# Kernel optimization log

Measured on AMD Instinct MI355X. Metric: run time of the kernel, lower is better.

Reference implementation:

```python
import jax, jax.numpy as jnp
import numpy as np

# SemiConv2d with semifield_type='MaxMin':
#   out[n,oc,i,j] = max_{ic,kh,kw} min(x_pad[n,ic,i+kh,j+kw], kernel[oc,ic,kh,kw])
# stride=1, 'same' padding with -inf (identity of max).

def setup_inputs() -> dict:
    key = jax.random.key(0)
    kx, kk = jax.random.split(key)
    x = jax.random.normal(kx, (8, 32, 96, 96), dtype=jnp.float32)
    kernel = jax.random.normal(kk, (32, 32, 3, 3), dtype=jnp.float32)
    return {"x": x, "kernel": kernel}


def reference(x, kernel):
    N, IC, H, W = x.shape
    OC, IC2, KH, KW = kernel.shape
    assert IC == IC2
    # same padding for k=3, stride=1 (left=top=1, right=bottom=1)
    p = KH - 1
    top = left = p // 2
    bot = right = p - top
    xp = jnp.pad(x, ((0, 0), (0, 0), (top, bot), (left, right)),
                 constant_values=-jnp.inf)
    out = None
    # small fixed loop over kernel taps (KH*KW = 9); vectorized over N, OC, IC, H, W
    for kh in range(KH):
        for kw in range(KW):
            win = xp[:, :, kh:kh + H, kw:kw + W]           # [N, IC, H, W]
            k_tap = kernel[:, :, kh, kw]                   # [OC, IC]
            # min over values, max over input channels -> [N, OC, H, W]
            v = jnp.max(jnp.minimum(win[:, None], k_tap[None, :, :, None, None]), axis=2)
            out = v if out is None else jnp.maximum(out, v)
    return out
```

## Files before the change

kernel.cpp:

```cpp
#include <hip/hip_runtime.h>
#include <math.h>
#include <stdint.h>


#define HH 96
#define WW 96
#define CIN 32
#define OCN 32
#define XQ_ROWS 98
#define ROWB 208
#define SLICEB (XQ_ROWS * ROWB)
#define XQ_BYTES ((size_t)256 * SLICEB)
#define ROWU4 13
#define XQP_TOTAL (256 * XQ_ROWS * ROWU4)
#define XQPB (XQP_TOTAL / 256)
#define NROW 96
#define TBL_BYTES ((size_t)OCN * NROW * 16)
#define RMX_BYTES ((size_t)OCN * NROW * 4)
#define WS_NEED (XQ_BYTES + TBL_BYTES + RMX_BYTES)
#define NEGH2 0xFC00FC00u

typedef _Float16 h2 __attribute__((ext_vector_type(2)));

__device__ __forceinline__ uint32_t pkmin_vs(uint32_t x, uint32_t k) {
    uint32_t d;
    asm("v_pk_min_f16 %0, %1, %2" : "=v"(d) : "v"(x), "s"(k));
    return d;
}
__device__ __forceinline__ uint32_t pkmin_vv(uint32_t a, uint32_t b) {
    uint32_t d;
    asm("v_pk_min_f16 %0, %1, %2" : "=v"(d) : "v"(a), "v"(b));
    return d;
}
__device__ __forceinline__ uint32_t pkmax(uint32_t a, uint32_t b) {
    uint32_t d;
    asm("v_pk_max_f16 %0, %1, %2" : "=v"(d) : "v"(a), "v"(b));
    return d;
}
__device__ __forceinline__ uint32_t packh2(float lo, float hi) {
    h2 p = {(_Float16)lo, (_Float16)hi};
    return __builtin_bit_cast(uint32_t, p);
}

__global__ __launch_bounds__(256) void setup_all(const float* __restrict__ x,
                                                 const float* __restrict__ kk,
                                                 uint4* __restrict__ xq,
                                                 uint4* __restrict__ tbl,
                                                 uint32_t* __restrict__ rmx) {
    __shared__ float rs[NROW];
    const int bb = blockIdx.x;
    if (bb < XQPB) {
        int idx = bb * 256 + threadIdx.x;
        int u  = idx % ROWU4;
        int t  = idx / ROWU4;
        int hp = t % XQ_ROWS;
        int s  = t / XQ_ROWS;
        int h  = hp - 1;
        bool hv = (h >= 0) && (h < HH);
        const float* row = x + ((size_t)s * HH + (hv ? h : 0)) * WW;
        float v[8];
#pragma unroll
        for (int q = 0; q < 8; ++q) {
            int w = 8 * u - 1 + q;
            v[q] = (hv && w >= 0 && w < WW) ? row[w] : -INFINITY;
        }
        uint4 o;
        o.x = packh2(v[0], v[1]);
        o.y = packh2(v[2], v[3]);
        o.z = packh2(v[4], v[5]);
        o.w = packh2(v[6], v[7]);
        xq[idx] = o;
        return;
    }
    const int oc = bb - XQPB;
    const int t  = threadIdx.x;
    if (t >= NROW) return;
    const int ic = t / 3, dh = t - 3 * ic;
    const float* kp = kk + ((size_t)(oc * CIN + ic) * 3 + dh) * 3;
    float k0 = kp[0], k1 = kp[1], k2 = kp[2];
    float rm = fmaxf(fmaxf(k0, k1), k2);
    rs[t] = rm;
    __syncthreads();
    int rank = 0;
    for (int s = 0; s < NROW; ++s) {
        float v = rs[s];
        rank += (v > rm) || (v == rm && s < t);
    }
    uint32_t off = (uint32_t)(ic * XQ_ROWS + dh) * ROWB;
    tbl[oc * NROW + rank] = make_uint4(packh2(k0, k0), packh2(k1, k1),
                                       packh2(k2, k2), off);
    rmx[oc * NROW + rank] = packh2(rm, rm);
}

__global__ __launch_bounds__(192, 8) void semiconv_w(const char* __restrict__ xqb,
                                                     const uint4* __restrict__ tbl,
                                                     const uint32_t* __restrict__ rmx,
                                                     float* __restrict__ out) {
    const int tid = threadIdx.x;
    const int wl = tid % 12;
    const int hh = tid / 12;
    const int b  = blockIdx.x;
    const int oc = b & 31;
    const int r  = b >> 5;
    const int hq = r % 6;
    const int n  = r / 6;
    const int h  = hq * 16 + hh;

    const char* xqn = xqb + (size_t)n * CIN * SLICEB;
    const int vb = h * ROWB + 16 * wl;
    const uint4* tb = tbl + oc * NROW;
    const uint32_t* rb = rmx + oc * NROW;

    uint32_t a0 = NEGH2, a1 = NEGH2, a2 = NEGH2, a3 = NEGH2;

    for (int c = 0; c < NROW / 2; ++c) {
        uint4 e0 = tb[2 * c], e1 = tb[2 * c + 1];
        uint32_t kn = (c < NROW / 2 - 1) ? rb[2 * c + 2] : 0u;

        const char* r0 = xqn + e0.w;
        const char* r1 = xqn + e1.w;
        uint4    d  = *(const uint4*)(r0 + vb);
        uint32_t d4 = *(const uint32_t*)(r0 + vb + 16);
        uint4    D  = *(const uint4*)(r1 + vb);
        uint32_t D4 = *(const uint32_t*)(r1 + vb + 16);

        uint32_t p01 = __builtin_amdgcn_alignbit(d.y, d.x, 16);
        uint32_t p12 = __builtin_amdgcn_alignbit(d.z, d.y, 16);
        uint32_t p23 = __builtin_amdgcn_alignbit(d.w, d.z, 16);
        uint32_t p34 = __builtin_amdgcn_alignbit(d4,  d.w, 16);
        a0 = pkmax(a0, pkmax(pkmax(pkmin_vs(d.x, e0.x), pkmin_vs(p01, e0.y)),
                             pkmin_vs(d.y, e0.z)));
        a1 = pkmax(a1, pkmax(pkmax(pkmin_vs(d.y, e0.x), pkmin_vs(p12, e0.y)),
                             pkmin_vs(d.z, e0.z)));
        a2 = pkmax(a2, pkmax(pkmax(pkmin_vs(d.z, e0.x), pkmin_vs(p23, e0.y)),
                             pkmin_vs(d.w, e0.z)));
        a3 = pkmax(a3, pkmax(pkmax(pkmin_vs(d.w, e0.x), pkmin_vs(p34, e0.y)),
                             pkmin_vs(d4,  e0.z)));
        uint32_t q01 = __builtin_amdgcn_alignbit(D.y, D.x, 16);
        uint32_t q12 = __builtin_amdgcn_alignbit(D.z, D.y, 16);
        uint32_t q23 = __builtin_amdgcn_alignbit(D.w, D.z, 16);
        uint32_t q34 = __builtin_amdgcn_alignbit(D4,  D.w, 16);
        a0 = pkmax(a0, pkmax(pkmax(pkmin_vs(D.x, e1.x), pkmin_vs(q01, e1.y)),
                             pkmin_vs(D.y, e1.z)));
        a1 = pkmax(a1, pkmax(pkmax(pkmin_vs(D.y, e1.x), pkmin_vs(q12, e1.y)),
                             pkmin_vs(D.z, e1.z)));
        a2 = pkmax(a2, pkmax(pkmax(pkmin_vs(D.z, e1.x), pkmin_vs(q23, e1.y)),
                             pkmin_vs(D.w, e1.z)));
        a3 = pkmax(a3, pkmax(pkmax(pkmin_vs(D.w, e1.x), pkmin_vs(q34, e1.y)),
                             pkmin_vs(D4,  e1.z)));

        if (c < NROW / 2 - 1) {
            uint32_t mn = pkmin_vv(pkmin_vv(a0, a1), pkmin_vv(a2, a3));
            mn = pkmin_vv(mn, __builtin_amdgcn_alignbit(mn, mn, 16));
            h2 a  = __builtin_bit_cast(h2, mn);
            h2 kv = __builtin_bit_cast(h2, kn);
            if (__all(a.x >= kv.x)) break;
        }
    }

    float* ob = out + (((size_t)(n * OCN + oc)) * HH + h) * WW + 8 * wl;
    h2 r0 = __builtin_bit_cast(h2, a0);
    h2 r1 = __builtin_bit_cast(h2, a1);
    h2 r2 = __builtin_bit_cast(h2, a2);
    h2 r3 = __builtin_bit_cast(h2, a3);
    float4 o1 = make_float4((float)r0.x, (float)r0.y, (float)r1.x, (float)r1.y);
    float4 o2 = make_float4((float)r2.x, (float)r2.y, (float)r3.x, (float)r3.y);
    *(float4*)(ob)     = o1;
    *(float4*)(ob + 4) = o2;
}

#define NEGINF (-INFINITY)
__global__ __launch_bounds__(192, 8) void semiconv2d_f32(
    const float* __restrict__ x, const float* __restrict__ kk, float* __restrict__ out)
{
    const int tid = threadIdx.x;
    const int w  = tid % WW;
    const int hr = tid / WW;
    const int b   = blockIdx.x;
    const int ocb = b & 7;
    const int hp  = (b >> 3) % 48;
    const int n   = (b >> 3) / 48;
    const int h   = hp * 2 + hr;
    const int oc0 = ocb * 4;
    float a0[4], a1[4], a2[4];
#pragma unroll
    for (int i = 0; i < 4; ++i) { a0[i] = NEGINF; a1[i] = NEGINF; a2[i] = NEGINF; }
    const bool vm = (h > 0), vp = (h < HH - 1);
    const int hm  = vm ? h - 1 : h;
    const int hpl = vp ? h + 1 : h;
    const int cm  = (w > 0) ? -1 : 0;
    const int cp  = (w < WW - 1) ? 1 : 0;
    const float* rm = x + ((size_t)(n * CIN) * HH + hm)  * WW + w;
    const float* r1 = x + ((size_t)(n * CIN) * HH + h)   * WW + w;
    const float* rp = x + ((size_t)(n * CIN) * HH + hpl) * WW + w;
#pragma unroll 2
    for (int ic = 0; ic < CIN; ++ic) {
        float r00 = vm ? rm[cm] : NEGINF, r01 = vm ? rm[0] : NEGINF, r02 = vm ? rm[cp] : NEGINF;
        float r10 = r1[cm], r11 = r1[0], r12 = r1[cp];
        float r20 = vp ? rp[cm] : NEGINF, r21 = vp ? rp[0] : NEGINF, r22 = vp ? rp[cp] : NEGINF;
#pragma unroll
        for (int oc = 0; oc < 4; ++oc) {
            const float* kq = kk + (size_t)(((oc0 + oc) * CIN + ic)) * 9;
            a0[oc] = fmaxf(fmaxf(a0[oc], fminf(r00, kq[0])), fmaxf(fminf(r10, kq[3]), fminf(r20, kq[6])));
            a1[oc] = fmaxf(fmaxf(a1[oc], fminf(r01, kq[1])), fmaxf(fminf(r11, kq[4]), fminf(r21, kq[7])));
            a2[oc] = fmaxf(fmaxf(a2[oc], fminf(r02, kq[2])), fmaxf(fminf(r12, kq[5]), fminf(r22, kq[8])));
        }
        rm += HH * WW; r1 += HH * WW; rp += HH * WW;
    }
#pragma unroll
    for (int oc = 0; oc < 4; ++oc) {
        float v0 = (w > 0)      ? a0[oc] : NEGINF;
        float v2 = (w < WW - 1) ? a2[oc] : NEGINF;
        out[(((size_t)(n * OCN + oc0 + oc)) * HH + h) * WW + w] = fmaxf(fmaxf(v0, a1[oc]), v2);
    }
}

extern "C" void kernel_launch(void* const* d_in, const int* in_sizes, int n_in,
                              void* d_out, int out_size, void* d_ws, size_t ws_size,
                              hipStream_t stream) {
    const float* x  = (const float*)d_in[0];
    const float* kk = (const float*)d_in[1];
    float* out      = (float*)d_out;
    if (ws_size >= WS_NEED) {
        uint4*    xq  = (uint4*)d_ws;
        uint4*    tbl = (uint4*)((char*)d_ws + XQ_BYTES);
        uint32_t* rmx = (uint32_t*)((char*)d_ws + XQ_BYTES + TBL_BYTES);
        setup_all<<<dim3(XQPB + OCN), dim3(256), 0, stream>>>(x, kk, xq, tbl, rmx);
        semiconv_w<<<dim3(8 * OCN * 6), dim3(192), 0, stream>>>(
            (const char*)xq, tbl, rmx, out);
    } else {
        semiconv2d_f32<<<dim3(8 * 48 * 8), dim3(192), 0, stream>>>(x, kk, out);
    }
}
```

Before: 88.16 us.

## Stage input row tile in LDS and share across eight output channels per block

The main kernel now cooperatively loads a 6-row by 32-channel slab of the fp16 padded input into shared memory, then has eight wavefronts (one per output channel) read their taps from LDS rather than from global memory. Each lane now computes 6 output columns instead of 8, and the block covers 4 rows, so the table offsets are rewritten to index the LDS slab. The aim is to cut repeated global/L2 traffic for the input across output channels. In exchange it adds a block-wide barrier and a 40KB LDS footprint, and the per-wave early-exit can leave waves idle while others finish.

Measured after the change: 86.69 us. No clear change (-1.7%).

```diff
diff --git a/kernel.cpp b/kernel.cpp
--- a/kernel.cpp
+++ b/kernel.cpp
@@ -9,9 +9,9 @@
 #define OCN 32
 #define XQ_ROWS 98
 #define ROWB 208
+#define ROWU4 13
 #define SLICEB (XQ_ROWS * ROWB)
 #define XQ_BYTES ((size_t)256 * SLICEB)
-#define ROWU4 13
 #define XQP_TOTAL (256 * XQ_ROWS * ROWU4)
 #define XQPB (XQP_TOTAL / 256)
 #define NROW 96
@@ -19,8 +19,10 @@
 #define RMX_BYTES ((size_t)OCN * NROW * 4)
 #define WS_NEED (XQ_BYTES + TBL_BYTES + RMX_BYTES)
 #define NEGH2 0xFC00FC00u
+#define LDSU 2496
 
 typedef _Float16 h2 __attribute__((ext_vector_type(2)));
+typedef uint32_t u4a4 __attribute__((ext_vector_type(4), aligned(4)));
 
 __device__ __forceinline__ uint32_t pkmin_vs(uint32_t x, uint32_t k) {
     uint32_t d;
@@ -86,71 +88,80 @@
         float v = rs[s];
         rank += (v > rm) || (v == rm && s < t);
     }
-    uint32_t off = (uint32_t)(ic * XQ_ROWS + dh) * ROWB;
+    uint32_t off = (uint32_t)(ic * 6 + dh) * ROWB;
     tbl[oc * NROW + rank] = make_uint4(packh2(k0, k0), packh2(k1, k1),
                                        packh2(k2, k2), off);
     rmx[oc * NROW + rank] = packh2(rm, rm);
 }
 
-__global__ __launch_bounds__(192, 8) void semiconv_w(const char* __restrict__ xqb,
-                                                     const uint4* __restrict__ tbl,
-                                                     const uint32_t* __restrict__ rmx,
-                                                     float* __restrict__ out) {
+__global__ __launch_bounds__(512, 4) void semiconv_lds(const char* __restrict__ xqb,
+                                                       const uint4* __restrict__ tbl,
+                                                       const uint32_t* __restrict__ rmx,
+                                                       float* __restrict__ out) {
+    __shared__ uint4 lsd[LDSU];
     const int tid = threadIdx.x;
-    const int wl = tid % 12;
-    const int hh = tid / 12;
-    const int b  = blockIdx.x;
-    const int oc = b & 31;
-    const int r  = b >> 5;
-    const int hq = r % 6;
-    const int n  = r / 6;
-    const int h  = hq * 16 + hh;
-
-    const char* xqn = xqb + (size_t)n * CIN * SLICEB;
-    const int vb = h * ROWB + 16 * wl;
+    const int b   = blockIdx.x;
+    const int ocl = b & 3;
+    const int t   = b >> 2;
+    const int ht  = t % 24;
+    const int n   = t / 24;
+    const int h0  = ht * 4;
+
+    const uint4* xg = (const uint4*)(xqb + (size_t)n * CIN * SLICEB);
+#pragma unroll
+    for (int i = 0; i < 5; ++i) {
+        int u = tid + 512 * i;
+        if (u < LDSU) {
+            int ic = u / 78;
+            int rr = u - ic * 78;
+            int r  = rr / 13;
+            int j  = rr - r * 13;
+            lsd[(ic * 6 + r) * 13 + j] = xg[(ic * 98 + h0 + r) * 13 + j];
+        }
+    }
+    __syncthreads();
+
+    const int lane = tid & 63;
+    const int oc   = ocl * 8 + (tid >> 6);
+    const int wl   = lane & 15;
+    const int hr   = lane >> 4;
+    const int h    = h0 + hr;
+    const char* ldsb = (const char*)lsd;
+    const int vb   = hr * ROWB + 12 * wl;
     const uint4* tb = tbl + oc * NROW;
     const uint32_t* rb = rmx + oc * NROW;
 
-    uint32_t a0 = NEGH2, a1 = NEGH2, a2 = NEGH2, a3 = NEGH2;
+    uint32_t a0 = NEGH2, a1 = NEGH2, a2 = NEGH2;
 
     for (int c = 0; c < NROW / 2; ++c) {
         uint4 e0 = tb[2 * c], e1 = tb[2 * c + 1];
         uint32_t kn = (c < NROW / 2 - 1) ? rb[2 * c + 2] : 0u;
 
-        const char* r0 = xqn + e0.w;
-        const char* r1 = xqn + e1.w;
-        uint4    d  = *(const uint4*)(r0 + vb);
-        uint32_t d4 = *(const uint32_t*)(r0 + vb + 16);
-        uint4    D  = *(const uint4*)(r1 + vb);
-        uint32_t D4 = *(const uint32_t*)(r1 + vb + 16);
+        u4a4 d = *(const u4a4*)(ldsb + e0.w + vb);
+        u4a4 D = *(const u4a4*)(ldsb + e1.w + vb);
 
         uint32_t p01 = __builtin_amdgcn_alignbit(d.y, d.x, 16);
         uint32_t p12 = __builtin_amdgcn_alignbit(d.z, d.y, 16);
         uint32_t p23 = __builtin_amdgcn_alignbit(d.w, d.z, 16);
-        uint32_t p34 = __builtin_amdgcn_alignbit(d4,  d.w, 16);
         a0 = pkmax(a0, pkmax(pkmax(pkmin_vs(d.x, e0.x), pkmin_vs(p01, e0.y)),
                              pkmin_vs(d.y, e0.z)));
         a1 = pkmax(a1, pkmax(pkmax(pkmin_vs(d.y, e0.x), pkmin_vs(p12, e0.y)),
                              pkmin_vs(d.z, e0.z)));
         a2 = pkmax(a2, pkmax(pkmax(pkmin_vs(d.z, e0.x), pkmin_vs(p23, e0.y)),
                              pkmin_vs(d.w, e0.z)));
-        a3 = pkmax(a3, pkmax(pkmax(pkmin_vs(d.w, e0.x), pkmin_vs(p34, e0.y)),
-                             pkmin_vs(d4,  e0.z)));
+
         uint32_t q01 = __builtin_amdgcn_alignbit(D.y, D.x, 16);
         uint32_t q12 = __builtin_amdgcn_alignbit(D.z, D.y, 16);
         uint32_t q23 = __builtin_amdgcn_alignbit(D.w, D.z, 16);
-        uint32_t q34 = __builtin_amdgcn_alignbit(D4,  D.w, 16);
         a0 = pkmax(a0, pkmax(pkmax(pkmin_vs(D.x, e1.x), pkmin_vs(q01, e1.y)),
                              pkmin_vs(D.y, e1.z)));
         a1 = pkmax(a1, pkmax(pkmax(pkmin_vs(D.y, e1.x), pkmin_vs(q12, e1.y)),
                              pkmin_vs(D.z, e1.z)));
         a2 = pkmax(a2, pkmax(pkmax(pkmin_vs(D.z, e1.x), pkmin_vs(q23, e1.y)),
                              pkmin_vs(D.w, e1.z)));
-        a3 = pkmax(a3, pkmax(pkmax(pkmin_vs(D.w, e1.x), pkmin_vs(q34, e1.y)),
-                             pkmin_vs(D4,  e1.z)));
 
         if (c < NROW / 2 - 1) {
-            uint32_t mn = pkmin_vv(pkmin_vv(a0, a1), pkmin_vv(a2, a3));
+            uint32_t mn = pkmin_vv(pkmin_vv(a0, a1), a2);
             mn = pkmin_vv(mn, __builtin_amdgcn_alignbit(mn, mn, 16));
             h2 a  = __builtin_bit_cast(h2, mn);
             h2 kv = __builtin_bit_cast(h2, kn);
@@ -158,15 +169,13 @@
         }
     }
 
-    float* ob = out + (((size_t)(n * OCN + oc)) * HH + h) * WW + 8 * wl;
+    float* ob = out + (((size_t)(n * OCN + oc)) * HH + h) * WW + 6 * wl;
     h2 r0 = __builtin_bit_cast(h2, a0);
     h2 r1 = __builtin_bit_cast(h2, a1);
     h2 r2 = __builtin_bit_cast(h2, a2);
-    h2 r3 = __builtin_bit_cast(h2, a3);
-    float4 o1 = make_float4((float)r0.x, (float)r0.y, (float)r1.x, (float)r1.y);
-    float4 o2 = make_float4((float)r2.x, (float)r2.y, (float)r3.x, (float)r3.y);
-    *(float4*)(ob)     = o1;
-    *(float4*)(ob + 4) = o2;
+    *(float2*)(ob)     = make_float2((float)r0.x, (float)r0.y);
+    *(float2*)(ob + 2) = make_float2((float)r1.x, (float)r1.y);
+    *(float2*)(ob + 4) = make_float2((float)r2.x, (float)r2.y);
 }
 
 #define NEGINF (-INFINITY)
@@ -226,7 +235,7 @@
         uint4*    tbl = (uint4*)((char*)d_ws + XQ_BYTES);
         uint32_t* rmx = (uint32_t*)((char*)d_ws + XQ_BYTES + TBL_BYTES);
         setup_all<<<dim3(XQPB + OCN), dim3(256), 0, stream>>>(x, kk, xq, tbl, rmx);
-        semiconv_w<<<dim3(8 * OCN * 6), dim3(192), 0, stream>>>(
+        semiconv_lds<<<dim3(4 * 24 * 8), dim3(512), 0, stream>>>(
             (const char*)xq, tbl, rmx, out);
     } else {
         semiconv2d_f32<<<dim3(8 * 48 * 8), dim3(192), 0, stream>>>(x, kk, out);
```
